# Kernel optimization log

Hardware: AMD Instinct MI355X
Metric: run time of the kernel (lower is better)

Reference implementation:

```python
import jax, jax.numpy as jnp
import numpy as np

B, D, OUT = 16384, 128, 32

def setup_inputs() -> dict:
    key = jax.random.key(0)
    kx, kw, kb = jax.random.split(key, 3)
    x = jax.random.normal(kx, (B, D), dtype=jnp.float32)
    # nn.Linear(in=D*(D+1), out=OUT): weight [OUT, D*(D+1)], bias [OUT]
    fan_in = D * (D + 1)
    bound = 1.0 / np.sqrt(fan_in)
    W = jax.random.uniform(kw, (OUT, fan_in), dtype=jnp.float32, minval=-bound, maxval=bound)
    b = jax.random.uniform(kb, (OUT,), dtype=jnp.float32, minval=-bound, maxval=bound)
    return {"x": x, "W": W, "b": b}

def reference(x, W, b):
    Bn, d = x.shape
    ones = jnp.ones((Bn, 1), dtype=x.dtype)
    xe = jnp.concatenate([x, ones], axis=-1)          # [B, d+1]
    # outer product z[b, i, j] = x[b, i] * xe[b, j]; flatten row-major -> [B, d*(d+1)]
    z = (x[:, :, None] * xe[:, None, :]).reshape(Bn, d * (d + 1))
    y = z @ W.T + b                                    # [B, OUT]
    return y
```

## Files before the change

### kernel.cpp

```cpp
#include <hip/hip_runtime.h>

typedef __attribute__((ext_vector_type(8)))  __bf16 bf16x8;
typedef __attribute__((ext_vector_type(4)))  __bf16 bf16x4;
typedef __attribute__((ext_vector_type(16))) float  f32x16;
typedef unsigned int uint32;

#define D_IN  128
#define N_OUT 32
#define K129  129
#define WROW  16512
#define KE    144
#define NT    8
#define XQ_ELEMS (16384 * 128)
#define WQ_ELEMS (32 * 128 * KE)

__global__ void prep(const float* __restrict__ x, const float* __restrict__ W,
                     __bf16* __restrict__ xq, __bf16* __restrict__ Wq) {
    int t = blockIdx.x * 256 + threadIdx.x;
    {
        const float4* s = reinterpret_cast<const float4*>(x) + (size_t)t * 2;
        float4 a = s[0], b = s[1];
        bf16x8 v = { (__bf16)a.x, (__bf16)a.y, (__bf16)a.z, (__bf16)a.w,
                     (__bf16)b.x, (__bf16)b.y, (__bf16)b.z, (__bf16)b.w };
        reinterpret_cast<bf16x8*>(xq)[t] = v;
    }
    for (int e = t; e < WQ_ELEMS; e += 262144) {
        int oi = e / KE, k = e - oi * KE;
        int o = oi >> 7, i = oi & 127;
        float v = (k <= D_IN) ? W[o * WROW + i * K129 + k] : 0.f;
        Wq[e] = (__bf16)v;
    }
}


#define STAGE(BUF, T)                                                              \
  do {                                                                             \
    if (PREP) {                                                                    \
      __builtin_amdgcn_global_load_lds(                                            \
        (const __attribute__((address_space(1))) uint32*)                          \
          (xq + ((rbase + (long)(T) * 32 + r0s) * D_IN + c0s * 8)),                \
        (__attribute__((address_space(3))) uint32*)(&tile[BUF][wave * 1024]),      \
        16, 0, 0);                                                                 \
      __builtin_amdgcn_global_load_lds(                                            \
        (const __attribute__((address_space(1))) uint32*)                          \
          (xq + ((rbase + (long)(T) * 32 + r1s) * D_IN + c1s * 8)),                \
        (__attribute__((address_space(3))) uint32*)(&tile[BUF][wave * 1024 + 512]),\
        16, 0, 0);                                                                 \
    } else {                                                                       \
      const float* s0 = x + (rbase + (long)(T) * 32 + r0s) * D_IN + c0s * 8;       \
      const float* s1 = x + (rbase + (long)(T) * 32 + r1s) * D_IN + c1s * 8;       \
      float4 a0 = *(const float4*)s0, a1 = *(const float4*)(s0 + 4);               \
      float4 b0 = *(const float4*)s1, b1 = *(const float4*)(s1 + 4);               \
      bf16x8 v0 = { (__bf16)a0.x,(__bf16)a0.y,(__bf16)a0.z,(__bf16)a0.w,           \
                    (__bf16)a1.x,(__bf16)a1.y,(__bf16)a1.z,(__bf16)a1.w };         \
      bf16x8 v1 = { (__bf16)b0.x,(__bf16)b0.y,(__bf16)b0.z,(__bf16)b0.w,           \
                    (__bf16)b1.x,(__bf16)b1.y,(__bf16)b1.z,(__bf16)b1.w };         \
      *(bf16x8*)&tile[BUF][(size_t)p0 * 8] = v0;                                   \
      *(bf16x8*)&tile[BUF][(size_t)p1 * 8] = v1;                                   \
    }                                                                              \
  } while (0)

#define COMPUTE(BUF, MT)                                                           \
  {                                                                                \
    const char* tb = (const char*)&tile[BUF][0];                                   \
    f32x16 a0, a1;                                                                 \
    _Pragma("unroll")                                                              \
    for (int r = 0; r < 16; ++r) { a0[r] = 0.f; a1[r] = 0.f; }                     \
    _Pragma("unroll")                                                              \
    for (int ks = 0; ks < 8; ++ks) {                                               \
      bf16x8 bfr = *reinterpret_cast<const bf16x8*>(tb + laneB[ks]);               \
      a0 = __builtin_amdgcn_mfma_f32_32x32x16_bf16(A[0][ks], bfr, a0, 0, 0, 0);    \
      a1 = __builtin_amdgcn_mfma_f32_32x32x16_bf16(A[1][ks], bfr, a1, 0, 0, 0);    \
    }                                                                              \
    a0 = __builtin_amdgcn_mfma_f32_32x32x16_bf16(A[0][8], B8c, a0, 0, 0, 0);       \
    a1 = __builtin_amdgcn_mfma_f32_32x32x16_bf16(A[1][8], B8c, a1, 0, 0, 0);       \
    bf16x4 xe0[4], xe1[4];                                                         \
    _Pragma("unroll")                                                              \
    for (int q = 0; q < 4; ++q) {                                                  \
      xe0[q] = *reinterpret_cast<const bf16x4*>(tb + laneX[0][q]);                 \
      xe1[q] = *reinterpret_cast<const bf16x4*>(tb + laneX[1][q]);                 \
    }                                                                              \
    float s0 = 0.f, s1 = 0.f;                                                      \
    _Pragma("unroll")                                                              \
    for (int q = 0; q < 4; ++q)                                                    \
      _Pragma("unroll")                                                            \
      for (int j = 0; j < 4; ++j) {                                                \
        s0 += a0[q * 4 + j] * (float)xe0[q][j];                                    \
        s1 += a1[q * 4 + j] * (float)xe1[q][j];                                    \
      }                                                                            \
    float s = s0 + s1;                                                             \
    s += __shfl_xor(s, 32);                                                        \
    sArr[MT] = s;                                                                  \
  }

template<int PREP>
__global__ __launch_bounds__(256, 2) void quad4(
    const float* __restrict__ x, const float* __restrict__ W,
    const __bf16* __restrict__ xq, const __bf16* __restrict__ Wq,
    const float* __restrict__ bias, float* __restrict__ out)
{
    __shared__ __align__(16) __bf16 tile[2][32 * 128];
    __shared__ float red[2][2][NT][32];

    const int tid  = threadIdx.x;
    const int lane = tid & 63;
    const int wave = tid >> 6;
    const int pairId = wave >> 1;
    const int sub  = wave & 1;
    const int b32  = lane & 31, hi = lane >> 5;

    const int bid = blockIdx.x;
    const int xcd = bid & 7, idx = bid >> 3;
    const int opair = idx & 15;
    const int run = xcd * 8 + (idx >> 4);
    const int o = opair * 2 + pairId;
    const long rbase = (long)run * (NT * 32);
    const float bias_o = bias[o];

    bf16x8 A[2][9];
    #pragma unroll
    for (int ct = 0; ct < 2; ++ct) {
        const int i = (sub * 2 + ct) * 32 + b32;
        if (PREP) {
            const __bf16* base = Wq + ((size_t)o * 128 + i) * KE + hi * 8;
            #pragma unroll
            for (int ks = 0; ks < 9; ++ks)
                A[ct][ks] = *reinterpret_cast<const bf16x8*>(base + ks * 16);
        } else {
            const float* wr = W + (size_t)o * WROW + (size_t)i * K129;
            #pragma unroll
            for (int ks = 0; ks < 8; ++ks) {
                bf16x8 f;
                #pragma unroll
                for (int r = 0; r < 8; ++r) f[r] = (__bf16)wr[ks * 16 + hi * 8 + r];
                A[ct][ks] = f;
            }
            bf16x8 f;
            #pragma unroll
            for (int r = 0; r < 8; ++r) f[r] = (__bf16)0.f;
            if (hi == 0) f[0] = (__bf16)wr[128];
            A[ct][8] = f;
        }
    }

    bf16x8 B8c;
    #pragma unroll
    for (int r = 0; r < 8; ++r) B8c[r] = (__bf16)0.f;
    if (hi == 0) B8c[0] = (__bf16)1.0f;

    const int p0 = wave * 128 + lane;
    const int r0s = p0 >> 4, c0s = (p0 & 15) ^ (r0s & 15);
    const int p1 = p0 + 64;
    const int r1s = p1 >> 4, c1s = (p1 & 15) ^ (r1s & 15);

    const int rm = b32 & 15;
    int laneB[8];
    #pragma unroll
    for (int ks = 0; ks < 8; ++ks)
        laneB[ks] = b32 * 256 + (((ks * 2 + hi) ^ rm) << 4);
    int laneX[2][4];
    #pragma unroll
    for (int ct = 0; ct < 2; ++ct)
        #pragma unroll
        for (int q = 0; q < 4; ++q)
            laneX[ct][q] = b32 * 256 + ((((sub * 2 + ct) * 4 + q) ^ rm) << 4) + hi * 8;

    float sArr[NT];

    STAGE(0, 0);
    __syncthreads();

    #pragma unroll
    for (int t2 = 0; t2 < NT / 2; ++t2) {
        if (t2 * 2 + 1 < NT) STAGE(1, t2 * 2 + 1);
        COMPUTE(0, t2 * 2);
        __syncthreads();
        if (t2 * 2 + 2 < NT) STAGE(0, t2 * 2 + 2);
        COMPUTE(1, t2 * 2 + 1);
        __syncthreads();
    }

    if (hi == 0) {
        #pragma unroll
        for (int mt = 0; mt < NT; ++mt) red[pairId][sub][mt][b32] = sArr[mt];
    }
    __syncthreads();
    if (sub == 0) {
        #pragma unroll
        for (int m = 0; m < NT / 2; ++m) {
            int mt = m * 2 + hi;
            out[(rbase + (long)mt * 32 + b32) * N_OUT + o] =
                red[pairId][0][mt][b32] + red[pairId][1][mt][b32] + bias_o;
        }
    }
}

extern "C" void kernel_launch(void* const* d_in, const int* in_sizes, int n_in,
                              void* d_out, int out_size, void* d_ws, size_t ws_size,
                              hipStream_t stream) {
    const float* x    = (const float*)d_in[0];
    const float* W    = (const float*)d_in[1];
    const float* bias = (const float*)d_in[2];
    float* out = (float*)d_out;

    const size_t need = (size_t)(XQ_ELEMS + WQ_ELEMS) * sizeof(__bf16);
    if (ws_size >= need) {
        __bf16* xq = (__bf16*)d_ws;
        __bf16* Wq = xq + XQ_ELEMS;
        prep<<<1024, 256, 0, stream>>>(x, W, xq, Wq);
        quad4<1><<<1024, 256, 0, stream>>>(x, W, xq, Wq, bias, out);
    } else {
        quad4<0><<<1024, 256, 0, stream>>>(x, W, (const __bf16*)nullptr,
                                           (const __bf16*)nullptr, bias, out);
    }
}
```

Measured before the change: 31.72 us.

## Give each wave a full output column and reuse B fragments for the epilogue

Each wave now computes all four 32-row chunks of i for one output o, so a block covers four outputs, the grid is halved and the cross-wave LDS reduction and its extra barrier go away. The W rows are permuted in prep (permSlot) so the MFMA accumulator layout lines up with the already-loaded B fragments. The epilogue's x multipliers then come from registers instead of separate LDS reads. This costs more register pressure (A grows to 4x9 bf16x8 per lane) and gives half as many blocks, which may lower occupancy or latency hiding.

New measurement: 27.79 us. -12.4%, faster.

```diff
diff --git a/kernel.cpp b/kernel.cpp
--- a/kernel.cpp
+++ b/kernel.cpp
@@ -1,7 +1,6 @@
 #include <hip/hip_runtime.h>
 
 typedef __attribute__((ext_vector_type(8)))  __bf16 bf16x8;
-typedef __attribute__((ext_vector_type(4)))  __bf16 bf16x4;
 typedef __attribute__((ext_vector_type(16))) float  f32x16;
 typedef unsigned int uint32;
 
@@ -13,6 +12,11 @@
 #define NT    8
 #define XQ_ELEMS (16384 * 128)
 #define WQ_ELEMS (32 * 128 * KE)
+
+__host__ __device__ __forceinline__ int permSlot(int s) {
+    int q = s >> 3, h = (s >> 2) & 1, j = s & 3;
+    return 16 * (q >> 1) + 8 * h + 4 * (q & 1) + j;
+}
 
 __global__ void prep(const float* __restrict__ x, const float* __restrict__ W,
                      __bf16* __restrict__ xq, __bf16* __restrict__ Wq) {
@@ -26,12 +30,12 @@
     }
     for (int e = t; e < WQ_ELEMS; e += 262144) {
         int oi = e / KE, k = e - oi * KE;
-        int o = oi >> 7, i = oi & 127;
+        int o = oi >> 7, sg = oi & 127;
+        int i = (sg & ~31) + permSlot(sg & 31);
         float v = (k <= D_IN) ? W[o * WROW + i * K129 + k] : 0.f;
         Wq[e] = (__bf16)v;
     }
 }
-
 
 #define STAGE(BUF, T)                                                              \
   do {                                                                             \
@@ -63,70 +67,62 @@
 #define COMPUTE(BUF, MT)                                                           \
   {                                                                                \
     const char* tb = (const char*)&tile[BUF][0];                                   \
-    f32x16 a0, a1;                                                                 \
+    bf16x8 Bf[8];                                                                  \
     _Pragma("unroll")                                                              \
-    for (int r = 0; r < 16; ++r) { a0[r] = 0.f; a1[r] = 0.f; }                     \
+    for (int ks = 0; ks < 8; ++ks)                                                 \
+      Bf[ks] = *reinterpret_cast<const bf16x8*>(tb + laneB[ks]);                   \
+    float s = 0.f;                                                                 \
     _Pragma("unroll")                                                              \
-    for (int ks = 0; ks < 8; ++ks) {                                               \
-      bf16x8 bfr = *reinterpret_cast<const bf16x8*>(tb + laneB[ks]);               \
-      a0 = __builtin_amdgcn_mfma_f32_32x32x16_bf16(A[0][ks], bfr, a0, 0, 0, 0);    \
-      a1 = __builtin_amdgcn_mfma_f32_32x32x16_bf16(A[1][ks], bfr, a1, 0, 0, 0);    \
+    for (int ct = 0; ct < 4; ++ct) {                                               \
+      f32x16 a;                                                                    \
+      _Pragma("unroll")                                                            \
+      for (int r = 0; r < 16; ++r) a[r] = 0.f;                                     \
+      _Pragma("unroll")                                                            \
+      for (int ks = 0; ks < 8; ++ks)                                               \
+        a = __builtin_amdgcn_mfma_f32_32x32x16_bf16(A[ct][ks], Bf[ks], a, 0, 0, 0);\
+      a = __builtin_amdgcn_mfma_f32_32x32x16_bf16(A[ct][8], B8c, a, 0, 0, 0);      \
+      _Pragma("unroll")                                                            \
+      for (int q = 0; q < 4; ++q)                                                  \
+        _Pragma("unroll")                                                          \
+        for (int j = 0; j < 4; ++j)                                                \
+          s += a[q * 4 + j] * (float)Bf[2 * ct + (q >> 1)][4 * (q & 1) + j];       \
     }                                                                              \
-    a0 = __builtin_amdgcn_mfma_f32_32x32x16_bf16(A[0][8], B8c, a0, 0, 0, 0);       \
-    a1 = __builtin_amdgcn_mfma_f32_32x32x16_bf16(A[1][8], B8c, a1, 0, 0, 0);       \
-    bf16x4 xe0[4], xe1[4];                                                         \
-    _Pragma("unroll")                                                              \
-    for (int q = 0; q < 4; ++q) {                                                  \
-      xe0[q] = *reinterpret_cast<const bf16x4*>(tb + laneX[0][q]);                 \
-      xe1[q] = *reinterpret_cast<const bf16x4*>(tb + laneX[1][q]);                 \
-    }                                                                              \
-    float s0 = 0.f, s1 = 0.f;                                                      \
-    _Pragma("unroll")                                                              \
-    for (int q = 0; q < 4; ++q)                                                    \
-      _Pragma("unroll")                                                            \
-      for (int j = 0; j < 4; ++j) {                                                \
-        s0 += a0[q * 4 + j] * (float)xe0[q][j];                                    \
-        s1 += a1[q * 4 + j] * (float)xe1[q][j];                                    \
-      }                                                                            \
-    float s = s0 + s1;                                                             \
     s += __shfl_xor(s, 32);                                                        \
-    sArr[MT] = s;                                                                  \
+    if (hi == 0)                                                                   \
+      out[(rbase + (long)(MT) * 32 + b32) * N_OUT + o] = s + bias_o;               \
   }
 
 template<int PREP>
-__global__ __launch_bounds__(256, 2) void quad4(
+__global__ __launch_bounds__(256, 2) void quad5(
     const float* __restrict__ x, const float* __restrict__ W,
     const __bf16* __restrict__ xq, const __bf16* __restrict__ Wq,
     const float* __restrict__ bias, float* __restrict__ out)
 {
     __shared__ __align__(16) __bf16 tile[2][32 * 128];
-    __shared__ float red[2][2][NT][32];
 
     const int tid  = threadIdx.x;
     const int lane = tid & 63;
     const int wave = tid >> 6;
-    const int pairId = wave >> 1;
-    const int sub  = wave & 1;
     const int b32  = lane & 31, hi = lane >> 5;
 
     const int bid = blockIdx.x;
     const int xcd = bid & 7, idx = bid >> 3;
-    const int opair = idx & 15;
-    const int run = xcd * 8 + (idx >> 4);
-    const int o = opair * 2 + pairId;
+    const int run = xcd * 8 + (idx & 7);
+    const int og  = idx >> 3;
+    const int o   = og * 4 + wave;
     const long rbase = (long)run * (NT * 32);
     const float bias_o = bias[o];
 
-    bf16x8 A[2][9];
+    bf16x8 A[4][9];
     #pragma unroll
-    for (int ct = 0; ct < 2; ++ct) {
-        const int i = (sub * 2 + ct) * 32 + b32;
+    for (int ct = 0; ct < 4; ++ct) {
         if (PREP) {
-            const __bf16* base = Wq + ((size_t)o * 128 + i) * KE + hi * 8;
+            const __bf16* base = Wq + ((size_t)o * 128 + ct * 32 + b32) * KE + hi * 8;
             #pragma unroll
             for (int ks = 0; ks < 9; ++ks)
                 A[ct][ks] = *reinterpret_cast<const bf16x8*>(base + ks * 16);
         } else {
+            const int i = ct * 32 + permSlot(b32);
             const float* wr = W + (size_t)o * WROW + (size_t)i * K129;
             #pragma unroll
             for (int ks = 0; ks < 8; ++ks) {
@@ -158,14 +154,6 @@
     #pragma unroll
     for (int ks = 0; ks < 8; ++ks)
         laneB[ks] = b32 * 256 + (((ks * 2 + hi) ^ rm) << 4);
-    int laneX[2][4];
-    #pragma unroll
-    for (int ct = 0; ct < 2; ++ct)
-        #pragma unroll
-        for (int q = 0; q < 4; ++q)
-            laneX[ct][q] = b32 * 256 + ((((sub * 2 + ct) * 4 + q) ^ rm) << 4) + hi * 8;
-
-    float sArr[NT];
 
     STAGE(0, 0);
     __syncthreads();
@@ -178,20 +166,6 @@
         if (t2 * 2 + 2 < NT) STAGE(0, t2 * 2 + 2);
         COMPUTE(1, t2 * 2 + 1);
         __syncthreads();
-    }
-
-    if (hi == 0) {
-        #pragma unroll
-        for (int mt = 0; mt < NT; ++mt) red[pairId][sub][mt][b32] = sArr[mt];
-    }
-    __syncthreads();
-    if (sub == 0) {
-        #pragma unroll
-        for (int m = 0; m < NT / 2; ++m) {
-            int mt = m * 2 + hi;
-            out[(rbase + (long)mt * 32 + b32) * N_OUT + o] =
-                red[pairId][0][mt][b32] + red[pairId][1][mt][b32] + bias_o;
-        }
     }
 }
 
@@ -208,9 +182,9 @@
         __bf16* xq = (__bf16*)d_ws;
         __bf16* Wq = xq + XQ_ELEMS;
         prep<<<1024, 256, 0, stream>>>(x, W, xq, Wq);
-        quad4<1><<<1024, 256, 0, stream>>>(x, W, xq, Wq, bias, out);
+        quad5<1><<<512, 256, 0, stream>>>(x, W, xq, Wq, bias, out);
     } else {
-        quad4<0><<<1024, 256, 0, stream>>>(x, W, (const __bf16*)nullptr,
-                                           (const __bf16*)nullptr, bias, out);
+        quad5<0><<<512, 256, 0, stream>>>(x, W, (const __bf16*)nullptr,
+                                          (const __bf16*)nullptr, bias, out);
     }
 }
```
